# Kernel tuning notes

Measured on AMD Instinct MI355X. Metric: run time of the kernel, lower is better.

## Reference

```python
import jax, jax.numpy as jnp
import numpy as np
from jax import lax

B, T, CD = 128, 4096, 2
HID, K = 64, 5
FIN = CD * 3 + 4  # 10 scorer input channels
PAD = K // 2
LEARNED_W = 0.5


def setup_inputs() -> dict:
    key = jax.random.key(0)
    ks = jax.random.split(key, 10)
    trajectory = jax.random.normal(ks[0], (B, T, CD), jnp.float32)
    intervals = jax.random.uniform(ks[1], (B, T), jnp.float32, 0.01, 1.0)
    lengths = jax.random.randint(ks[2], (B,), T // 2, T + 1)
    attention_mask = (jnp.arange(T)[None, :] < lengths[:, None]).astype(jnp.float32)
    observed_mask = (jax.random.uniform(ks[3], (B, T)) > 0.3).astype(jnp.float32)
    w1 = jax.random.normal(ks[4], (HID, FIN, K), jnp.float32) / np.sqrt(FIN * K)
    b1 = jnp.zeros((HID,), jnp.float32)
    w2 = jax.random.normal(ks[5], (HID, HID, K), jnp.float32) / np.sqrt(HID * K)
    b2 = jnp.zeros((HID,), jnp.float32)
    w3 = jax.random.normal(ks[6], (1, HID, 1), jnp.float32) / np.sqrt(HID)
    b3 = jnp.zeros((1,), jnp.float32)
    return dict(trajectory=trajectory, intervals=intervals, attention_mask=attention_mask,
                observed_mask=observed_mask, w1=w1, b1=b1, w2=w2, b2=b2, w3=w3, b3=b3)


def _conv1d(x, w, pad):  # x: [B,C,T], w: [O,I,K]
    return lax.conv_general_dilated(x, w, (1,), [(pad, pad)],
                                    dimension_numbers=('NCH', 'OIH', 'NCH'))


def _safe_norm(v):  # grad-safe L2 norm over last dim, exact forward
    s2 = jnp.sum(v * v, axis=-1)
    return jnp.where(s2 > 0, jnp.sqrt(jnp.where(s2 > 0, s2, 1.0)), 0.0)


def _robust_normalize(values, mask):
    # vectorized version of per-sample 95th-percentile scaling
    valid = mask > 0.5
    n = jnp.sum(valid, axis=1)  # [B] int
    s = jnp.sort(jnp.where(valid, values, jnp.inf), axis=1)  # valid ascending, inf last
    idx = jnp.maximum(1, jnp.ceil(n.astype(jnp.float32) * 0.95).astype(jnp.int32)) - 1
    idx = jnp.clip(idx, 0, T - 1)
    scale = jnp.abs(jnp.take_along_axis(s, idx[:, None], axis=1))[:, 0]
    maxabs = jnp.max(jnp.where(valid, jnp.abs(values), 0.0), axis=1)
    scale = jnp.where(scale < 1e-6, maxabs, scale)
    out = values / jnp.maximum(scale, 1e-6)[:, None]
    out = jnp.where((n > 0)[:, None], out, 0.0)
    return out * mask


def _smooth(scores, mask):  # avg_pool1d k=K stride 1 pad K//2 (count_include_pad=True)
    kern = jnp.full((1, 1, K), 1.0 / K, scores.dtype)
    sm = _conv1d(scores[:, None, :], kern, PAD)[:, 0]
    return sm * mask


def _forward(trajectory, intervals, attention_mask, observed_mask, w1, b1, w2, b2, w3, b3):
    mask = attention_mask
    vm = mask > 0.5
    pm = (vm[:, 1:] & vm[:, :-1]).astype(trajectory.dtype)  # [B,T-1]

    def mdiff3(x):
        d = (x[:, 1:] - x[:, :-1]) * pm[..., None]
        return jnp.concatenate([jnp.zeros_like(x[:, :1]), d], axis=1)

    def mdiff2(x):
        d = (x[:, 1:] - x[:, :-1]) * pm
        return jnp.concatenate([jnp.zeros_like(x[:, :1]), d], axis=1)

    mt = trajectory * mask[..., None]
    coord_diff = mdiff3(mt)
    delta_t = jnp.maximum(intervals[..., None], 1e-3)
    interval_feat = intervals * mask
    velocity = coord_diff / delta_t * mask[..., None]
    acceleration = mdiff3(velocity) / delta_t * mask[..., None]
    speed = _safe_norm(velocity) * mask
    speed_change = jnp.abs(mdiff2(speed)) * mask
    accel_norm = _safe_norm(acceleration) * mask
    heading = jnp.arctan2(velocity[..., 1], velocity[..., 0])
    rhc = heading[:, 1:] - heading[:, :-1]
    rhc = jnp.abs(jnp.arctan2(jnp.sin(rhc), jnp.cos(rhc)))
    heading_change = jnp.concatenate([jnp.zeros_like(speed[:, :1]), rhc * pm], axis=1) * mask
    obs_feat = observed_mask * mask
    ot = jnp.abs(observed_mask[:, 1:] - observed_mask[:, :-1]) * pm
    observed_transition = jnp.concatenate([jnp.zeros_like(speed[:, :1]), ot], axis=1) * mask

    feats = jnp.concatenate([mt, velocity, acceleration, speed[..., None],
                             heading_change[..., None], interval_feat[..., None],
                             obs_feat[..., None]], axis=-1) * mask[..., None]  # [B,T,10]

    # rule scores
    scores = (0.35 * _robust_normalize(heading_change, mask)
              + 0.30 * _robust_normalize(accel_norm, mask)
              + 0.25 * _robust_normalize(speed_change, mask)
              + 0.10 * jnp.clip(observed_transition, 0.0, 1.0) * mask)
    scores = _smooth(scores, mask)
    rule_scores = jnp.clip(_robust_normalize(scores, mask), 0.0, 1.0) * mask

    # learned scores (Conv1d stack, exact GELU like torch default)
    x = feats.transpose(0, 2, 1)  # [B,10,T]
    h = jax.nn.gelu(_conv1d(x, w1, PAD) + b1[None, :, None], approximate=False)
    h = jax.nn.gelu(_conv1d(h, w2, PAD) + b2[None, :, None], approximate=False)
    learned = jax.nn.sigmoid((_conv1d(h, w3, 0) + b3[None, :, None])[:, 0]) * mask
    learned = jnp.clip(_smooth(learned, mask), 0.0, 1.0)

    out = (1.0 - LEARNED_W) * rule_scores + LEARNED_W * learned
    return jnp.clip(out, 0.0, 1.0) * mask


def reference(trajectory, intervals, attention_mask, observed_mask, w1, b1, w2, b2, w3, b3):
    return _forward(trajectory, intervals, attention_mask, observed_mask, w1, b1, w2, b2, w3, b3)
```

## Files before the change

kernel.cpp:

```cpp
#include <hip/hip_runtime.h>

namespace {

constexpr int B_ = 128;
constexpr int T_ = 4096;
constexpr int BT = B_ * T_;
constexpr int TTILE = 128;
constexpr unsigned NOINS = 0xFFFFFFFFu;

constexpr size_t OFF_W1F   = 0;
constexpr size_t OFF_W2F   = 2048;
constexpr size_t OFF_FEATS = 16384;
constexpr size_t OFF_HC    = OFF_FEATS + (size_t)B_ * 10 * T_;
constexpr size_t OFF_AN    = OFF_HC + (size_t)BT;
constexpr size_t OFF_SC    = OFF_AN + (size_t)BT;
constexpr size_t OFF_OT    = OFF_SC + (size_t)BT;
constexpr size_t OFF_RULE  = OFF_OT + (size_t)BT;
constexpr size_t OFF_LP    = OFF_RULE + (size_t)BT;

typedef _Float16 half8 __attribute__((ext_vector_type(8)));
typedef _Float16 half4 __attribute__((ext_vector_type(4)));
typedef _Float16 half2_t __attribute__((ext_vector_type(2)));
typedef float f32x4 __attribute__((ext_vector_type(4)));

__device__ __forceinline__ float clip01(float x) { return fminf(fmaxf(x, 0.f), 1.f); }

__device__ __forceinline__ float gelu_fast(float x) {
  float s = x * 0.7071067811865475f;
  float a = fabsf(s);
  float t = __builtin_amdgcn_rcpf(__builtin_fmaf(0.3275911f, a, 1.0f));
  float p = __builtin_fmaf(t, 1.061405429f, -1.453152027f);
  p = __builtin_fmaf(t, p, 1.421413741f);
  p = __builtin_fmaf(t, p, -0.284496736f);
  p = __builtin_fmaf(t, p, 0.254829592f);
  p = p * t;
  float e = __builtin_amdgcn_exp2f(a * a * -1.4426950408889634f);
  float erfa = __builtin_fmaf(-p, e, 1.0f);
  float erfs = copysignf(erfa, s);
  return 0.5f * x * (1.0f + erfs);
}

__device__ __forceinline__ void compute_feats(
    const float* __restrict__ tr, const float* __restrict__ iv,
    const float* __restrict__ mk, const float* __restrict__ om, int t,
    float* __restrict__ f , float* anv_out, float* scv_out, float* otv_out) {
  float m  = mk[t];
  float m1 = (t >= 1) ? mk[t - 1] : 0.f;
  float m2 = (t >= 2) ? mk[t - 2] : 0.f;
  float pm01 = (m > 0.5f && m1 > 0.5f) ? 1.f : 0.f;
  float pm12 = (m1 > 0.5f && m2 > 0.5f) ? 1.f : 0.f;
  float x0x = tr[2 * t] * m, x0y = tr[2 * t + 1] * m;
  float x1x = 0.f, x1y = 0.f, x2x = 0.f, x2y = 0.f;
  if (t >= 1) { x1x = tr[2 * (t - 1)] * m1; x1y = tr[2 * (t - 1) + 1] * m1; }
  if (t >= 2) { x2x = tr[2 * (t - 2)] * m2; x2y = tr[2 * (t - 2) + 1] * m2; }
  float dt0 = fmaxf(iv[t], 1e-3f);
  float dt1 = (t >= 1) ? fmaxf(iv[t - 1], 1e-3f) : 1e-3f;
  float vx = 0.f, vy = 0.f, v1x = 0.f, v1y = 0.f;
  if (t >= 1) { vx = (x0x - x1x) * pm01 / dt0 * m; vy = (x0y - x1y) * pm01 / dt0 * m; }
  if (t >= 2) { v1x = (x1x - x2x) * pm12 / dt1 * m1; v1y = (x1y - x2y) * pm12 / dt1 * m1; }
  float ax = 0.f, ay = 0.f;
  if (t >= 1) { ax = (vx - v1x) * pm01 / dt0 * m; ay = (vy - v1y) * pm01 / dt0 * m; }
  float s2 = vx * vx + vy * vy;
  float speed = (s2 > 0.f ? sqrtf(s2) : 0.f) * m;
  float s21 = v1x * v1x + v1y * v1y;
  float speed1 = (s21 > 0.f ? sqrtf(s21) : 0.f) * m1;
  float scv = (t >= 1) ? fabsf((speed - speed1) * pm01) * m : 0.f;
  float a2 = ax * ax + ay * ay;
  float anv = (a2 > 0.f ? sqrtf(a2) : 0.f) * m;
  float hcv = 0.f;
  if (t >= 1) {
    bool z0 = (vx == 0.f && vy == 0.f);
    bool z1 = (v1x == 0.f && v1y == 0.f);
    float yy, xx;
    if (z1)      { yy = vy;  xx = vx; }
    else if (z0) { yy = v1y; xx = v1x; }
    else { yy = vy * v1x - vx * v1y; xx = vx * v1x + vy * v1y; }
    hcv = fabsf(atan2f(yy, xx)) * pm01 * m;
  }
  float obs = om[t] * m;
  float otv = (t >= 1) ? fminf(fabsf(om[t] - om[t - 1]) * pm01 * m, 1.f) : 0.f;
  float itf = iv[t] * m;
  f[0] = x0x; f[1] = x0y; f[2] = vx; f[3] = vy; f[4] = ax; f[5] = ay;
  f[6] = speed; f[7] = hcv; f[8] = itf; f[9] = obs;
  *anv_out = anv; *scv_out = scv; *otv_out = otv;
}

__global__ __launch_bounds__(256)
void featurize_k(const float* __restrict__ traj, const float* __restrict__ intervals,
                 const float* __restrict__ amask, const float* __restrict__ omask,
                 const float* __restrict__ w1g, const float* __restrict__ w2g,
                 float* __restrict__ feats, float* __restrict__ hc, float* __restrict__ an,
                 float* __restrict__ sc, float* __restrict__ ot,
                 half8* __restrict__ w1f, half8* __restrict__ w2f) {
  int idx = blockIdx.x * 256 + threadIdx.x;
  int b = idx >> 12;
  int t = idx & (T_ - 1);
  float f[10], anv, scv, otv;
  compute_feats(traj + (size_t)b * T_ * 2, intervals + (size_t)b * T_,
                amask + (size_t)b * T_, omask + (size_t)b * T_, t, f, &anv, &scv, &otv);
  float* frow = feats + (size_t)b * 10 * T_;
#pragma unroll
  for (int c = 0; c < 10; ++c) frow[(size_t)c * T_ + t] = f[c];
  hc[idx] = f[7]; an[idx] = anv; sc[idx] = scv; ot[idx] = otv;

  if (blockIdx.x < 12) {
    int gid = blockIdx.x * 256 + threadIdx.x;
    if (gid < 48 * 64) {
      int fid = gid >> 6, lane = gid & 63;
      int qd = lane >> 4, ln = lane & 15;
      half8 v;
      if (fid < 8) {
        int m = fid >> 1, kk = fid & 1;
        int o = m * 16 + ln;
#pragma unroll
        for (int j = 0; j < 8; ++j) {
          int ck = kk * 32 + qd * 8 + j;
          float val = 0.f;
          if (ck < 50) { int k_ = ck / 10, c = ck - 10 * k_; val = w1g[o * 50 + c * 5 + k_]; }
          v[j] = (_Float16)val;
        }
        w1f[fid * 64 + lane] = v;
      } else {
        int f2 = fid - 8;
        int k = f2 >> 3, kk = (f2 >> 2) & 1, m = f2 & 3;
        int o = m * 16 + ln;
#pragma unroll
        for (int j = 0; j < 8; ++j) {
          int ic = kk * 32 + qd * 8 + j;
          v[j] = (_Float16)w2g[o * 320 + ic * 5 + k];
        }
        w2f[f2 * 64 + lane] = v;
      }
    }
  }
}

template <int CHUNK, int NB>
__device__ __forceinline__ void find_bucket_1k(const unsigned* __restrict__ hist,
                                               unsigned* selb, unsigned* selk,
                                               unsigned* sW, int tid) {
  unsigned k = *selk;
  unsigned vals[CHUNK];
  unsigned ps = 0;
#pragma unroll
  for (int c = 0; c < CHUNK; ++c) {
    int idx = tid * CHUNK + c;
    unsigned v = (idx < NB) ? hist[idx] : 0u;
    vals[c] = v; ps += v;
  }
  unsigned incl = ps;
  int lane = tid & 63;
#pragma unroll
  for (int off = 1; off < 64; off <<= 1) {
    unsigned tv = __shfl_up(incl, off, 64);
    if (lane >= off) incl += tv;
  }
  if (lane == 63) sW[tid >> 6] = incl;
  __syncthreads();
  int wid = tid >> 6;
  unsigned woff = 0;
  for (int i = 0; i < wid; ++i) woff += sW[i];
  incl += woff;
  unsigned excl = incl - ps;
  __syncthreads();
  if (excl <= k && k < incl) {
    unsigned run = excl;
    int c = 0;
#pragma unroll
    for (; c < CHUNK - 1; ++c) {
      if (run + vals[c] > k) break;
      run += vals[c];
    }
    *selb = (unsigned)(tid * CHUNK + c);
    *selk = k - run;
  }
  __syncthreads();
}

__device__ __forceinline__ float radix_select_1k(const unsigned* u, unsigned k,
                                                 unsigned* hist, unsigned* selb,
                                                 unsigned* selk, unsigned* sW, int tid) {
  for (int i = tid; i < 4096; i += 1024) hist[i] = 0u;
  if (tid == 0) *selk = k;
  __syncthreads();
#pragma unroll
  for (int r = 0; r < 4; ++r)
    if (u[r] != NOINS) atomicAdd(&hist[u[r] >> 20], 1u);
  __syncthreads();
  find_bucket_1k<4, 4096>(hist, selb, selk, sW, tid);
  unsigned p1 = *selb;
  for (int i = tid; i < 4096; i += 1024) hist[i] = 0u;
  __syncthreads();
#pragma unroll
  for (int r = 0; r < 4; ++r)
    if (u[r] != NOINS && (u[r] >> 20) == p1) atomicAdd(&hist[(u[r] >> 8) & 0xFFFu], 1u);
  __syncthreads();
  find_bucket_1k<4, 4096>(hist, selb, selk, sW, tid);
  unsigned p2 = *selb;
  unsigned pref = (p1 << 12) | p2;
  if (tid < 256) hist[tid] = 0u;
  __syncthreads();
#pragma unroll
  for (int r = 0; r < 4; ++r)
    if (u[r] != NOINS && (u[r] >> 8) == pref) atomicAdd(&hist[u[r] & 0xFFu], 1u);
  __syncthreads();
  find_bucket_1k<1, 256>(hist, selb, selk, sW, tid);
  unsigned p3 = *selb;
  __syncthreads();
  return __uint_as_float((p1 << 20) | (p2 << 8) | p3);
}

__device__ __forceinline__ float block_max_1k(float v, float* sM, int tid) {
#pragma unroll
  for (int off = 32; off; off >>= 1) v = fmaxf(v, __shfl_xor(v, off));
  if ((tid & 63) == 0) sM[tid >> 6] = v;
  __syncthreads();
  float m = sM[0];
#pragma unroll
  for (int i = 1; i < 16; ++i) m = fmaxf(m, sM[i]);
  __syncthreads();
  return m;
}

__global__ __launch_bounds__(1024)
void ruleselect_k(const float* __restrict__ hc, const float* __restrict__ an,
                  const float* __restrict__ sc, const float* __restrict__ ot,
                  const float* __restrict__ amask, float* __restrict__ rule) {
  __shared__ unsigned hist[4096];
  __shared__ unsigned sW[16];
  __shared__ unsigned selb, selk;
  __shared__ float vbuf[4096];
  __shared__ float sM[16];
  __shared__ int iCnt[16];
  __shared__ int n_sh;
  __shared__ float scale_sh[3];
  int b = blockIdx.x, tid = threadIdx.x;
  const float* mk = amask + (size_t)b * T_;
  const float* hrow = hc + (size_t)b * T_;
  const float* arow = an + (size_t)b * T_;
  const float* srow = sc + (size_t)b * T_;
  const float* orow = ot + (size_t)b * T_;

  float hcv[4], anv[4], scv[4], otv[4], mreg[4];
  int cnt = 0;
#pragma unroll
  for (int r = 0; r < 4; ++r) {
    int t = tid + 1024 * r;
    hcv[r] = hrow[t]; anv[r] = arow[t]; scv[r] = srow[t]; otv[r] = orow[t];
    mreg[r] = mk[t];
    cnt += (mreg[r] > 0.5f);
  }
#pragma unroll
  for (int off = 32; off; off >>= 1) cnt += __shfl_xor(cnt, off);
  if ((tid & 63) == 0) iCnt[tid >> 6] = cnt;
  __syncthreads();
  if (tid == 0) {
    int n = 0;
#pragma unroll
    for (int i = 0; i < 16; ++i) n += iCnt[i];
    n_sh = n;
  }
  __syncthreads();
  int n = n_sh;
  int cidx = (int)ceilf((float)n * 0.95f);
  if (cidx < 1) cidx = 1;
  int kidx = cidx - 1;
  if (kidx < 0) kidx = 0;
  if (kidx > T_ - 1) kidx = T_ - 1;

  for (int m3 = 0; m3 < 3; ++m3) {
    unsigned u[4];
    float mx = 0.f;
#pragma unroll
    for (int r = 0; r < 4; ++r) {
      float v = (m3 == 0 ? hcv[r] : m3 == 1 ? anv[r] : scv[r]);
      if (mreg[r] > 0.5f) {
        mx = fmaxf(mx, fabsf(v));
        unsigned ub = __float_as_uint(v);
        if ((int)ub < 0) ub = 0u;
        u[r] = ub;
      } else u[r] = NOINS;
    }
    mx = block_max_1k(mx, sM, tid);
    float kth = fabsf(radix_select_1k(u, (unsigned)kidx, hist, &selb, &selk, sW, tid));
    if (tid == 0) {
      float s = (kth < 1e-6f) ? mx : kth;
      scale_sh[m3] = fmaxf(s, 1e-6f);
    }
  }
  __syncthreads();
  float sc0 = scale_sh[0], sc1 = scale_sh[1], sc2 = scale_sh[2];
#pragma unroll
  for (int r = 0; r < 4; ++r) {
    int t = tid + 1024 * r;
    float v = 0.f;
    if (n > 0) {
      v = 0.35f * (hcv[r] / sc0) + 0.30f * (anv[r] / sc1)
        + 0.25f * (scv[r] / sc2) + 0.10f * otv[r];
    }
    vbuf[t] = v;
  }
  __syncthreads();
  float sm[4];
#pragma unroll
  for (int r = 0; r < 4; ++r) {
    int t = tid + 1024 * r;
    float s = 0.f;
#pragma unroll
    for (int d = -2; d <= 2; ++d) {
      int tt = t + d;
      if (tt >= 0 && tt < T_) s += vbuf[tt];
    }
    sm[r] = s * 0.2f * mreg[r];
  }
  unsigned u2[4];
  float mx2 = 0.f;
#pragma unroll
  for (int r = 0; r < 4; ++r) {
    if (mreg[r] > 0.5f) {
      mx2 = fmaxf(mx2, fabsf(sm[r]));
      unsigned ub = __float_as_uint(sm[r]);
      if ((int)ub < 0) ub = 0u;
      u2[r] = ub;
    } else u2[r] = NOINS;
  }
  mx2 = block_max_1k(mx2, sM, tid);
  float kth4 = fabsf(radix_select_1k(u2, (unsigned)kidx, hist, &selb, &selk, sW, tid));
  float scale4 = fmaxf((kth4 < 1e-6f) ? mx2 : kth4, 1e-6f);
  float* rrow = rule + (size_t)b * T_;
#pragma unroll
  for (int r = 0; r < 4; ++r) {
    int t = tid + 1024 * r;
    float v = (n > 0) ? sm[r] / scale4 : 0.f;
    rrow[t] = clip01(v) * mreg[r];
  }
}

__global__ __launch_bounds__(512, 4)
void conv_k(const float* __restrict__ feats, const half8* __restrict__ w1f,
            const float* __restrict__ b1g, const half8* __restrict__ w2f,
            const float* __restrict__ b2g, const float* __restrict__ w3g,
            const float* __restrict__ b3g, const float* __restrict__ amask,
            float* __restrict__ lp) {
  __shared__ _Float16 sIm[144 * 72];
  __shared__ _Float16 sH1[132 * 72];
  __shared__ float sF[10 * 136];
  __shared__ float sPart[2][128];
  int tid = threadIdx.x;
  int lane = tid & 63, w = tid >> 6;
  int qd = lane >> 4, ln = lane & 15;
  int tile = blockIdx.x, b = blockIdx.y;
  int t0 = tile * TTILE;
  const float* frow = feats + (size_t)b * 10 * T_;

  for (int s = tid; s < 1360; s += 512) {
    int c = s / 136, u = s - c * 136;
    int t = t0 - 4 + u;
    sF[s] = (t >= 0 && t < T_) ? frow[(size_t)c * T_ + t] * 0.015625f : 0.f;
  }
  for (int s = tid; s < 144 * 7; s += 512) {
    int jt = s / 7, d = s - jt * 7;
    *reinterpret_cast<unsigned*>(&sIm[jt * 72 + 50 + 2 * d]) = 0u;
  }
  __syncthreads();
  for (int s = tid; s < 660; s += 512) {
    int jt = s / 5, k = s - jt * 5;
#pragma unroll
    for (int cp = 0; cp < 5; ++cp) {
      float lo = sF[(2 * cp) * 136 + jt + k];
      float hi = sF[(2 * cp + 1) * 136 + jt + k];
      half2_t pk;
      pk[0] = (_Float16)lo;
      pk[1] = (_Float16)hi;
      *reinterpret_cast<half2_t*>(&sIm[jt * 72 + k * 10 + 2 * cp]) = pk;
    }
  }
  __syncthreads();

  half8 a1[4][2];
#pragma unroll
  for (int m = 0; m < 4; ++m)
#pragma unroll
    for (int kk = 0; kk < 2; ++kk) a1[m][kk] = w1f[(m * 2 + kk) * 64 + lane];

  for (int n0 = w; n0 < 9; n0 += 8) {
    int jt = n0 * 16 + ln;
    half8 bf0 = *reinterpret_cast<const half8*>(&sIm[jt * 72 + qd * 8]);
    half8 bf1 = *reinterpret_cast<const half8*>(&sIm[jt * 72 + 32 + qd * 8]);
#pragma unroll
    for (int m = 0; m < 4; ++m) {
      f32x4 acc;
      f32x4 bv = *reinterpret_cast<const f32x4*>(&b1g[m * 16 + qd * 4]);
#pragma unroll
      for (int r = 0; r < 4; ++r) acc[r] = bv[r] * 0.015625f;
      acc = __builtin_amdgcn_mfma_f32_16x16x32_f16(a1[m][0], bf0, acc, 0, 0, 0);
      acc = __builtin_amdgcn_mfma_f32_16x16x32_f16(a1[m][1], bf1, acc, 0, 0, 0);
      if (jt < 132) {
        int t = t0 - 2 + jt;
        bool inr = (t >= 0 && t < T_);
        half4 hv;
#pragma unroll
        for (int r = 0; r < 4; ++r) {
          float h = inr ? gelu_fast(acc[r] * 64.f) * 0.0625f : 0.f;
          hv[r] = (_Float16)h;
        }
        *reinterpret_cast<half4*>(&sH1[jt * 72 + m * 16 + qd * 4]) = hv;
      }
    }
  }
  __syncthreads();

  int p = w & 1, nq = w >> 1;
  f32x4 acc2[2][2];
#pragma unroll
  for (int dm = 0; dm < 2; ++dm) {
    f32x4 bv = *reinterpret_cast<const f32x4*>(&b2g[(2 * p + dm) * 16 + qd * 4]);
#pragma unroll
    for (int dn = 0; dn < 2; ++dn)
#pragma unroll
      for (int r = 0; r < 4; ++r) acc2[dm][dn][r] = bv[r] * 0.0625f;
  }
#pragma unroll
  for (int k = 0; k < 5; ++k) {
#pragma unroll
    for (int kk = 0; kk < 2; ++kk) {
      half8 A0 = w2f[((k * 2 + kk) * 4 + 2 * p + 0) * 64 + lane];
      half8 A1 = w2f[((k * 2 + kk) * 4 + 2 * p + 1) * 64 + lane];
      half8 B0 = *reinterpret_cast<const half8*>(
          &sH1[((2 * nq + 0) * 16 + ln + k) * 72 + kk * 32 + qd * 8]);
      half8 B1 = *reinterpret_cast<const half8*>(
          &sH1[((2 * nq + 1) * 16 + ln + k) * 72 + kk * 32 + qd * 8]);
      acc2[0][0] = __builtin_amdgcn_mfma_f32_16x16x32_f16(A0, B0, acc2[0][0], 0, 0, 0);
      acc2[0][1] = __builtin_amdgcn_mfma_f32_16x16x32_f16(A0, B1, acc2[0][1], 0, 0, 0);
      acc2[1][0] = __builtin_amdgcn_mfma_f32_16x16x32_f16(A1, B0, acc2[1][0], 0, 0, 0);
      acc2[1][1] = __builtin_amdgcn_mfma_f32_16x16x32_f16(A1, B1, acc2[1][1], 0, 0, 0);
    }
  }
  f32x4 w3a = *reinterpret_cast<const f32x4*>(&w3g[(2 * p + 0) * 16 + qd * 4]);
  f32x4 w3b = *reinterpret_cast<const f32x4*>(&w3g[(2 * p + 1) * 16 + qd * 4]);
#pragma unroll
  for (int dn = 0; dn < 2; ++dn) {
    float s = 0.f;
#pragma unroll
    for (int r = 0; r < 4; ++r) s += w3a[r] * gelu_fast(acc2[0][dn][r] * 16.f);
#pragma unroll
    for (int r = 0; r < 4; ++r) s += w3b[r] * gelu_fast(acc2[1][dn][r] * 16.f);
    s += __shfl_xor(s, 16);
    s += __shfl_xor(s, 32);
    if (lane < 16) sPart[p][(2 * nq + dn) * 16 + lane] = s;
  }
  __syncthreads();
  if (tid < 128) {
    int t = t0 + tid;
    float logit = sPart[0][tid] + sPart[1][tid] + b3g[0];
    float m = amask[(size_t)b * T_ + t];
    lp[(size_t)b * T_ + t] = (1.f / (1.f + expf(-logit))) * m;
  }
}

__global__ __launch_bounds__(256)
void final_k(const float* __restrict__ rule, const float* __restrict__ lp,
             const float* __restrict__ amask, float* __restrict__ out) {
  int idx = blockIdx.x * 256 + threadIdx.x;
  if (idx >= BT) return;
  int t = idx & (T_ - 1);
  float s = 0.f;
#pragma unroll
  for (int d = -2; d <= 2; ++d) {
    int tt = t + d;
    if (tt >= 0 && tt < T_) s += lp[idx + d];
  }
  float m = amask[idx];
  float learned = clip01(s * 0.2f * m);
  out[idx] = clip01(0.5f * rule[idx] + 0.5f * learned) * m;
}

}

extern "C" void kernel_launch(void* const* d_in, const int* in_sizes, int n_in,
                              void* d_out, int out_size, void* d_ws, size_t ws_size,
                              hipStream_t stream) {
  const float* traj      = (const float*)d_in[0];
  const float* intervals = (const float*)d_in[1];
  const float* amask     = (const float*)d_in[2];
  const float* omask     = (const float*)d_in[3];
  const float* w1        = (const float*)d_in[4];
  const float* b1        = (const float*)d_in[5];
  const float* w2        = (const float*)d_in[6];
  const float* b2        = (const float*)d_in[7];
  const float* w3        = (const float*)d_in[8];
  const float* b3        = (const float*)d_in[9];
  float* out = (float*)d_out;
  float* ws = (float*)d_ws;

  float* feats = ws + OFF_FEATS;
  float* hc    = ws + OFF_HC;
  float* an    = ws + OFF_AN;
  float* sc    = ws + OFF_SC;
  float* ot    = ws + OFF_OT;
  float* rule  = ws + OFF_RULE;
  float* lp    = ws + OFF_LP;
  half8* w1f = (half8*)(ws + OFF_W1F);
  half8* w2f = (half8*)(ws + OFF_W2F);

  featurize_k<<<BT / 256, 256, 0, stream>>>(traj, intervals, amask, omask, w1, w2,
                                            feats, hc, an, sc, ot, w1f, w2f);
  ruleselect_k<<<B_, 1024, 0, stream>>>(hc, an, sc, ot, amask, rule);
  conv_k<<<dim3(T_ / TTILE, B_), 512, 0, stream>>>(feats, w1f, b1, w2f, b2, w3, b3,
                                                   amask, lp);
  final_k<<<BT / 256, 256, 0, stream>>>(rule, lp, amask, out);
}
```

Measured before the change: 181.7 us.

## Batch three radix selects into shared passes and fuse histogram zeroing into scans

The rule-score kernel previously ran three sequential radix-select passes, each with its own block max and many barriers. Now the three metrics get separate histograms that are built and scanned together, and the scans zero the histogram as they read it, so separate clear loops and many __syncthreads go away. The cost is 48KB of shared histograms plus vbuf, which may lower occupancy, and higher register pressure from holding three metrics at once.

```diff
diff --git a/kernel.cpp b/kernel.cpp
--- a/kernel.cpp
+++ b/kernel.cpp
@@ -135,168 +135,205 @@
   }
 }
 
-template <int CHUNK, int NB>
-__device__ __forceinline__ void find_bucket_1k(const unsigned* __restrict__ hist,
-                                               unsigned* selb, unsigned* selk,
-                                               unsigned* sW, int tid) {
-  unsigned k = *selk;
-  unsigned vals[CHUNK];
-  unsigned ps = 0;
-#pragma unroll
-  for (int c = 0; c < CHUNK; ++c) {
-    int idx = tid * CHUNK + c;
-    unsigned v = (idx < NB) ? hist[idx] : 0u;
-    vals[c] = v; ps += v;
-  }
-  unsigned incl = ps;
-  int lane = tid & 63;
+__device__ __forceinline__ void scan4096(unsigned (*hist)[4096], int j, int tid, int lane,
+                                         int wv, unsigned (*sW)[16], uint4& v,
+                                         unsigned& ps, unsigned& incl) {
+  v = *reinterpret_cast<uint4*>(&hist[j][tid * 4]);
+  uint4 zz = {0u, 0u, 0u, 0u};
+  *reinterpret_cast<uint4*>(&hist[j][tid * 4]) = zz;
+  ps = v.x + v.y + v.z + v.w;
+  incl = ps;
 #pragma unroll
   for (int off = 1; off < 64; off <<= 1) {
     unsigned tv = __shfl_up(incl, off, 64);
     if (lane >= off) incl += tv;
   }
-  if (lane == 63) sW[tid >> 6] = incl;
-  __syncthreads();
-  int wid = tid >> 6;
+  if (lane == 63) sW[j][wv] = incl;
+}
+__device__ __forceinline__ void resolve4096(const unsigned (*sW)[16], int j, int tid, int wv,
+                                            uint4 v, unsigned ps, unsigned incl, unsigned k,
+                                            unsigned* selb, unsigned* selk) {
   unsigned woff = 0;
-  for (int i = 0; i < wid; ++i) woff += sW[i];
+  for (int i = 0; i < wv; ++i) woff += sW[j][i];
   incl += woff;
   unsigned excl = incl - ps;
-  __syncthreads();
   if (excl <= k && k < incl) {
+    unsigned vv[4] = {v.x, v.y, v.z, v.w};
     unsigned run = excl;
     int c = 0;
 #pragma unroll
-    for (; c < CHUNK - 1; ++c) {
-      if (run + vals[c] > k) break;
-      run += vals[c];
-    }
-    *selb = (unsigned)(tid * CHUNK + c);
+    for (; c < 3; ++c) {
+      if (run + vv[c] > k) break;
+      run += vv[c];
+    }
+    *selb = (unsigned)(tid * 4 + c);
     *selk = k - run;
   }
-  __syncthreads();
-}
-
-__device__ __forceinline__ float radix_select_1k(const unsigned* u, unsigned k,
-                                                 unsigned* hist, unsigned* selb,
-                                                 unsigned* selk, unsigned* sW, int tid) {
-  for (int i = tid; i < 4096; i += 1024) hist[i] = 0u;
-  if (tid == 0) *selk = k;
-  __syncthreads();
-#pragma unroll
-  for (int r = 0; r < 4; ++r)
-    if (u[r] != NOINS) atomicAdd(&hist[u[r] >> 20], 1u);
-  __syncthreads();
-  find_bucket_1k<4, 4096>(hist, selb, selk, sW, tid);
-  unsigned p1 = *selb;
-  for (int i = tid; i < 4096; i += 1024) hist[i] = 0u;
-  __syncthreads();
-#pragma unroll
-  for (int r = 0; r < 4; ++r)
-    if (u[r] != NOINS && (u[r] >> 20) == p1) atomicAdd(&hist[(u[r] >> 8) & 0xFFFu], 1u);
-  __syncthreads();
-  find_bucket_1k<4, 4096>(hist, selb, selk, sW, tid);
-  unsigned p2 = *selb;
-  unsigned pref = (p1 << 12) | p2;
-  if (tid < 256) hist[tid] = 0u;
-  __syncthreads();
-#pragma unroll
-  for (int r = 0; r < 4; ++r)
-    if (u[r] != NOINS && (u[r] >> 8) == pref) atomicAdd(&hist[u[r] & 0xFFu], 1u);
-  __syncthreads();
-  find_bucket_1k<1, 256>(hist, selb, selk, sW, tid);
-  unsigned p3 = *selb;
-  __syncthreads();
-  return __uint_as_float((p1 << 20) | (p2 << 8) | p3);
-}
-
-__device__ __forceinline__ float block_max_1k(float v, float* sM, int tid) {
-#pragma unroll
-  for (int off = 32; off; off >>= 1) v = fmaxf(v, __shfl_xor(v, off));
-  if ((tid & 63) == 0) sM[tid >> 6] = v;
-  __syncthreads();
-  float m = sM[0];
-#pragma unroll
-  for (int i = 1; i < 16; ++i) m = fmaxf(m, sM[i]);
-  __syncthreads();
-  return m;
+}
+__device__ __forceinline__ void scan256(unsigned (*hist)[4096], int j, int tid, int lane,
+                                        int wv, unsigned (*sW)[16], unsigned& v,
+                                        unsigned& incl) {
+  v = (tid < 256) ? hist[j][tid] : 0u;
+  if (tid < 256) hist[j][tid] = 0u;
+  incl = v;
+#pragma unroll
+  for (int off = 1; off < 64; off <<= 1) {
+    unsigned tv = __shfl_up(incl, off, 64);
+    if (lane >= off) incl += tv;
+  }
+  if (lane == 63) sW[j][wv] = incl;
+}
+__device__ __forceinline__ void resolve256(const unsigned (*sW)[16], int j, int tid, int wv,
+                                           unsigned v, unsigned incl, unsigned k,
+                                           unsigned* selb) {
+  unsigned woff = 0;
+  for (int i = 0; i < wv; ++i) woff += sW[j][i];
+  incl += woff;
+  unsigned excl = incl - v;
+  if (excl <= k && k < incl) *selb = (unsigned)tid;
 }
 
 __global__ __launch_bounds__(1024)
 void ruleselect_k(const float* __restrict__ hc, const float* __restrict__ an,
                   const float* __restrict__ sc, const float* __restrict__ ot,
                   const float* __restrict__ amask, float* __restrict__ rule) {
-  __shared__ unsigned hist[4096];
-  __shared__ unsigned sW[16];
-  __shared__ unsigned selb, selk;
+  __shared__ unsigned hist3[3][4096];
   __shared__ float vbuf[4096];
-  __shared__ float sM[16];
+  __shared__ unsigned selB[2][4];
+  __shared__ unsigned selK[2][4];
+  __shared__ unsigned sW3[3][16];
+  __shared__ float sM3[3][16];
   __shared__ int iCnt[16];
-  __shared__ int n_sh;
-  __shared__ float scale_sh[3];
   int b = blockIdx.x, tid = threadIdx.x;
+  int lane = tid & 63, wv = tid >> 6;
   const float* mk = amask + (size_t)b * T_;
-  const float* hrow = hc + (size_t)b * T_;
-  const float* arow = an + (size_t)b * T_;
-  const float* srow = sc + (size_t)b * T_;
-  const float* orow = ot + (size_t)b * T_;
-
-  float hcv[4], anv[4], scv[4], otv[4], mreg[4];
+  const float* h0 = hc + (size_t)b * T_;
+  const float* a0 = an + (size_t)b * T_;
+  const float* s0 = sc + (size_t)b * T_;
+  const float* o0 = ot + (size_t)b * T_;
+
+  float mv0[4], mv1[4], mv2[4], otv[4], mreg[4];
   int cnt = 0;
 #pragma unroll
   for (int r = 0; r < 4; ++r) {
     int t = tid + 1024 * r;
-    hcv[r] = hrow[t]; anv[r] = arow[t]; scv[r] = srow[t]; otv[r] = orow[t];
+    mv0[r] = h0[t]; mv1[r] = a0[t]; mv2[r] = s0[t]; otv[r] = o0[t];
     mreg[r] = mk[t];
     cnt += (mreg[r] > 0.5f);
   }
 #pragma unroll
   for (int off = 32; off; off >>= 1) cnt += __shfl_xor(cnt, off);
-  if ((tid & 63) == 0) iCnt[tid >> 6] = cnt;
-  __syncthreads();
-  if (tid == 0) {
-    int n = 0;
-#pragma unroll
-    for (int i = 0; i < 16; ++i) n += iCnt[i];
-    n_sh = n;
-  }
-  __syncthreads();
-  int n = n_sh;
+  if (lane == 0) iCnt[wv] = cnt;
+  {
+    unsigned* hflat = &hist3[0][0];
+    for (int i = tid; i < 3 * 4096; i += 1024) hflat[i] = 0u;
+  }
+  unsigned u0[4], u1[4], u2[4];
+  float mxa = 0.f, mxb = 0.f, mxc = 0.f;
+#pragma unroll
+  for (int r = 0; r < 4; ++r) {
+    bool valid = mreg[r] > 0.5f;
+    unsigned b0 = __float_as_uint(mv0[r]); if ((int)b0 < 0) b0 = 0u;
+    unsigned b1 = __float_as_uint(mv1[r]); if ((int)b1 < 0) b1 = 0u;
+    unsigned b2 = __float_as_uint(mv2[r]); if ((int)b2 < 0) b2 = 0u;
+    u0[r] = valid ? b0 : NOINS;
+    u1[r] = valid ? b1 : NOINS;
+    u2[r] = valid ? b2 : NOINS;
+    if (valid) {
+      mxa = fmaxf(mxa, fabsf(mv0[r]));
+      mxb = fmaxf(mxb, fabsf(mv1[r]));
+      mxc = fmaxf(mxc, fabsf(mv2[r]));
+    }
+  }
+#pragma unroll
+  for (int off = 32; off; off >>= 1) {
+    mxa = fmaxf(mxa, __shfl_xor(mxa, off));
+    mxb = fmaxf(mxb, __shfl_xor(mxb, off));
+    mxc = fmaxf(mxc, __shfl_xor(mxc, off));
+  }
+  if (lane == 0) { sM3[0][wv] = mxa; sM3[1][wv] = mxb; sM3[2][wv] = mxc; }
+  __syncthreads();
+  int n = 0;
+#pragma unroll
+  for (int i = 0; i < 16; ++i) n += iCnt[i];
   int cidx = (int)ceilf((float)n * 0.95f);
   if (cidx < 1) cidx = 1;
-  int kidx = cidx - 1;
-  if (kidx < 0) kidx = 0;
-  if (kidx > T_ - 1) kidx = T_ - 1;
-
-  for (int m3 = 0; m3 < 3; ++m3) {
-    unsigned u[4];
-    float mx = 0.f;
-#pragma unroll
-    for (int r = 0; r < 4; ++r) {
-      float v = (m3 == 0 ? hcv[r] : m3 == 1 ? anv[r] : scv[r]);
-      if (mreg[r] > 0.5f) {
-        mx = fmaxf(mx, fabsf(v));
-        unsigned ub = __float_as_uint(v);
-        if ((int)ub < 0) ub = 0u;
-        u[r] = ub;
-      } else u[r] = NOINS;
-    }
-    mx = block_max_1k(mx, sM, tid);
-    float kth = fabsf(radix_select_1k(u, (unsigned)kidx, hist, &selb, &selk, sW, tid));
-    if (tid == 0) {
-      float s = (kth < 1e-6f) ? mx : kth;
-      scale_sh[m3] = fmaxf(s, 1e-6f);
-    }
-  }
-  __syncthreads();
-  float sc0 = scale_sh[0], sc1 = scale_sh[1], sc2 = scale_sh[2];
+  unsigned kidx = (unsigned)(cidx - 1);
+  if (kidx > (unsigned)(T_ - 1)) kidx = T_ - 1;
+  float mx3a = sM3[0][0], mx3b = sM3[1][0], mx3c = sM3[2][0];
+#pragma unroll
+  for (int i = 1; i < 16; ++i) {
+    mx3a = fmaxf(mx3a, sM3[0][i]);
+    mx3b = fmaxf(mx3b, sM3[1][i]);
+    mx3c = fmaxf(mx3c, sM3[2][i]);
+  }
+
+#pragma unroll
+  for (int r = 0; r < 4; ++r) {
+    if (u0[r] != NOINS) atomicAdd(&hist3[0][u0[r] >> 20], 1u);
+    if (u1[r] != NOINS) atomicAdd(&hist3[1][u1[r] >> 20], 1u);
+    if (u2[r] != NOINS) atomicAdd(&hist3[2][u2[r] >> 20], 1u);
+  }
+  __syncthreads();
+  uint4 v40, v41, v42; unsigned ps0, ps1, ps2, in0, in1, in2;
+  scan4096(hist3, 0, tid, lane, wv, sW3, v40, ps0, in0);
+  scan4096(hist3, 1, tid, lane, wv, sW3, v41, ps1, in1);
+  scan4096(hist3, 2, tid, lane, wv, sW3, v42, ps2, in2);
+  __syncthreads();
+  resolve4096(sW3, 0, tid, wv, v40, ps0, in0, kidx, &selB[1][0], &selK[1][0]);
+  resolve4096(sW3, 1, tid, wv, v41, ps1, in1, kidx, &selB[1][1], &selK[1][1]);
+  resolve4096(sW3, 2, tid, wv, v42, ps2, in2, kidx, &selB[1][2], &selK[1][2]);
+  __syncthreads();
+  unsigned p1_0 = selB[1][0], p1_1 = selB[1][1], p1_2 = selB[1][2];
+  unsigned k2_0 = selK[1][0], k2_1 = selK[1][1], k2_2 = selK[1][2];
+#pragma unroll
+  for (int r = 0; r < 4; ++r) {
+    if (u0[r] != NOINS && (u0[r] >> 20) == p1_0) atomicAdd(&hist3[0][(u0[r] >> 8) & 0xFFFu], 1u);
+    if (u1[r] != NOINS && (u1[r] >> 20) == p1_1) atomicAdd(&hist3[1][(u1[r] >> 8) & 0xFFFu], 1u);
+    if (u2[r] != NOINS && (u2[r] >> 20) == p1_2) atomicAdd(&hist3[2][(u2[r] >> 8) & 0xFFFu], 1u);
+  }
+  __syncthreads();
+  scan4096(hist3, 0, tid, lane, wv, sW3, v40, ps0, in0);
+  scan4096(hist3, 1, tid, lane, wv, sW3, v41, ps1, in1);
+  scan4096(hist3, 2, tid, lane, wv, sW3, v42, ps2, in2);
+  __syncthreads();
+  resolve4096(sW3, 0, tid, wv, v40, ps0, in0, k2_0, &selB[0][0], &selK[0][0]);
+  resolve4096(sW3, 1, tid, wv, v41, ps1, in1, k2_1, &selB[0][1], &selK[0][1]);
+  resolve4096(sW3, 2, tid, wv, v42, ps2, in2, k2_2, &selB[0][2], &selK[0][2]);
+  __syncthreads();
+  unsigned p2_0 = selB[0][0], p2_1 = selB[0][1], p2_2 = selB[0][2];
+  unsigned k3_0 = selK[0][0], k3_1 = selK[0][1], k3_2 = selK[0][2];
+  unsigned pf0 = (p1_0 << 12) | p2_0, pf1 = (p1_1 << 12) | p2_1, pf2 = (p1_2 << 12) | p2_2;
+#pragma unroll
+  for (int r = 0; r < 4; ++r) {
+    if (u0[r] != NOINS && (u0[r] >> 8) == pf0) atomicAdd(&hist3[0][u0[r] & 0xFFu], 1u);
+    if (u1[r] != NOINS && (u1[r] >> 8) == pf1) atomicAdd(&hist3[1][u1[r] & 0xFFu], 1u);
+    if (u2[r] != NOINS && (u2[r] >> 8) == pf2) atomicAdd(&hist3[2][u2[r] & 0xFFu], 1u);
+  }
+  __syncthreads();
+  unsigned s80, s81, s82;
+  scan256(hist3, 0, tid, lane, wv, sW3, s80, in0);
+  scan256(hist3, 1, tid, lane, wv, sW3, s81, in1);
+  scan256(hist3, 2, tid, lane, wv, sW3, s82, in2);
+  __syncthreads();
+  resolve256(sW3, 0, tid, wv, s80, in0, k3_0, &selB[1][0]);
+  resolve256(sW3, 1, tid, wv, s81, in1, k3_1, &selB[1][1]);
+  resolve256(sW3, 2, tid, wv, s82, in2, k3_2, &selB[1][2]);
+  __syncthreads();
+  float kth0 = fabsf(__uint_as_float((p1_0 << 20) | (p2_0 << 8) | selB[1][0]));
+  float kth1 = fabsf(__uint_as_float((p1_1 << 20) | (p2_1 << 8) | selB[1][1]));
+  float kth2 = fabsf(__uint_as_float((p1_2 << 20) | (p2_2 << 8) | selB[1][2]));
+  float sc0 = fmaxf((kth0 < 1e-6f) ? mx3a : kth0, 1e-6f);
+  float sc1 = fmaxf((kth1 < 1e-6f) ? mx3b : kth1, 1e-6f);
+  float sc2 = fmaxf((kth2 < 1e-6f) ? mx3c : kth2, 1e-6f);
+
 #pragma unroll
   for (int r = 0; r < 4; ++r) {
     int t = tid + 1024 * r;
     float v = 0.f;
     if (n > 0) {
-      v = 0.35f * (hcv[r] / sc0) + 0.30f * (anv[r] / sc1)
-        + 0.25f * (scv[r] / sc2) + 0.10f * otv[r];
+      v = 0.35f * (mv0[r] / sc0) + 0.30f * (mv1[r] / sc1)
+        + 0.25f * (mv2[r] / sc2) + 0.10f * otv[r];
     }
     vbuf[t] = v;
   }
@@ -313,20 +350,50 @@
     }
     sm[r] = s * 0.2f * mreg[r];
   }
-  unsigned u2[4];
-  float mx2 = 0.f;
-#pragma unroll
-  for (int r = 0; r < 4; ++r) {
-    if (mreg[r] > 0.5f) {
-      mx2 = fmaxf(mx2, fabsf(sm[r]));
-      unsigned ub = __float_as_uint(sm[r]);
-      if ((int)ub < 0) ub = 0u;
-      u2[r] = ub;
-    } else u2[r] = NOINS;
-  }
-  mx2 = block_max_1k(mx2, sM, tid);
-  float kth4 = fabsf(radix_select_1k(u2, (unsigned)kidx, hist, &selb, &selk, sW, tid));
-  float scale4 = fmaxf((kth4 < 1e-6f) ? mx2 : kth4, 1e-6f);
+  unsigned uu[4];
+  float mxs = 0.f;
+#pragma unroll
+  for (int r = 0; r < 4; ++r) {
+    bool valid = mreg[r] > 0.5f;
+    unsigned ub = __float_as_uint(sm[r]); if ((int)ub < 0) ub = 0u;
+    uu[r] = valid ? ub : NOINS;
+    if (valid) mxs = fmaxf(mxs, fabsf(sm[r]));
+  }
+#pragma unroll
+  for (int off = 32; off; off >>= 1) mxs = fmaxf(mxs, __shfl_xor(mxs, off));
+  if (lane == 0) sM3[0][wv] = mxs;
+#pragma unroll
+  for (int r = 0; r < 4; ++r)
+    if (uu[r] != NOINS) atomicAdd(&hist3[0][uu[r] >> 20], 1u);
+  __syncthreads();
+  float mx4 = sM3[0][0];
+#pragma unroll
+  for (int i = 1; i < 16; ++i) mx4 = fmaxf(mx4, sM3[0][i]);
+  scan4096(hist3, 0, tid, lane, wv, sW3, v40, ps0, in0);
+  __syncthreads();
+  resolve4096(sW3, 0, tid, wv, v40, ps0, in0, kidx, &selB[1][3], &selK[1][3]);
+  __syncthreads();
+  unsigned q1 = selB[1][3], kq2 = selK[1][3];
+#pragma unroll
+  for (int r = 0; r < 4; ++r)
+    if (uu[r] != NOINS && (uu[r] >> 20) == q1) atomicAdd(&hist3[0][(uu[r] >> 8) & 0xFFFu], 1u);
+  __syncthreads();
+  scan4096(hist3, 0, tid, lane, wv, sW3, v40, ps0, in0);
+  __syncthreads();
+  resolve4096(sW3, 0, tid, wv, v40, ps0, in0, kq2, &selB[0][3], &selK[0][3]);
+  __syncthreads();
+  unsigned q2 = selB[0][3], kq3 = selK[0][3];
+  unsigned qf = (q1 << 12) | q2;
+#pragma unroll
+  for (int r = 0; r < 4; ++r)
+    if (uu[r] != NOINS && (uu[r] >> 8) == qf) atomicAdd(&hist3[0][uu[r] & 0xFFu], 1u);
+  __syncthreads();
+  scan256(hist3, 0, tid, lane, wv, sW3, s80, in0);
+  __syncthreads();
+  resolve256(sW3, 0, tid, wv, s80, in0, kq3, &selB[1][3]);
+  __syncthreads();
+  float kth4 = fabsf(__uint_as_float((q1 << 20) | (q2 << 8) | selB[1][3]));
+  float scale4 = fmaxf((kth4 < 1e-6f) ? mx4 : kth4, 1e-6f);
   float* rrow = rule + (size_t)b * T_;
 #pragma unroll
   for (int r = 0; r < 4; ++r) {
```

Result: no change. 178.8 us (-1.6%).
